# Kernel tuning notes

Measured on AMD Instinct MI355X. Metric: run time of the kernel, lower is better.

Reference implementation:

```python
import jax, jax.numpy as jnp
import numpy as np

N = 100000       # nodes
F_IN = 1433      # input features (Cora)
HID = 67         # hidden dim (hardcoded in module)
C = 7            # classes (Cora)
E = 3200000      # edges (avg degree 32)


def setup_inputs() -> dict:
    key = jax.random.key(0)
    k = jax.random.split(key, 4)
    x = jax.random.normal(k[0], (N, F_IN), dtype=jnp.float32)
    edge_index = jax.random.randint(k[1], (2, E), 0, N, dtype=jnp.int32)
    W1 = jax.random.normal(k[2], (F_IN, HID), dtype=jnp.float32) / np.float32(np.sqrt(F_IN))
    b1 = jnp.zeros((HID,), dtype=jnp.float32)
    W2 = jax.random.normal(k[3], (HID, C), dtype=jnp.float32) / np.float32(np.sqrt(HID))
    b2 = jnp.zeros((C,), dtype=jnp.float32)
    return {"x": x, "edge_index": edge_index, "W1": W1, "b1": b1, "W2": W2, "b2": b2}


def gcn_conv(x, edge_index, W, b):
    """PyG GCNConv: h = W x; out = D^-1/2 (A + I) D^-1/2 h + b."""
    n = x.shape[0]
    h = x @ W  # [n, out_dim]
    loops = jnp.arange(n, dtype=edge_index.dtype)
    row = jnp.concatenate([edge_index[0], loops])  # source
    col = jnp.concatenate([edge_index[1], loops])  # target
    deg = jax.ops.segment_sum(jnp.ones_like(col, dtype=h.dtype), col, num_segments=n)
    dinv = jnp.where(deg > 0, jax.lax.rsqrt(deg), jnp.float32(0))
    norm = dinv[row] * dinv[col]                    # [E+n]
    msg = h[row] * norm[:, None]                    # gather + scale
    out = jax.ops.segment_sum(msg, col, num_segments=n)  # scatter-add
    return out + b


def reference(x, edge_index, W1, b1, W2, b2):
    h = gcn_conv(x, edge_index, W1, b1)
    h = jax.nn.leaky_relu(h, negative_slope=0.01)
    # F.dropout(p=0.951, training=self.training) -> identity in eval mode
    h = gcn_conv(h, edge_index, W2, b2)
    return jax.nn.log_softmax(h, axis=1)
```

## Files before the change

### kernel.cpp

```cpp
#include <hip/hip_runtime.h>
#include <math.h>

#define FIN  1433
#define HID  67
#define HIDP 68
#define NC   7
#define NCP  8

#define BK     32
#define KTILES 45
#define KPAD   (KTILES*BK)
#define COLP   80

typedef __attribute__((ext_vector_type(8))) short short8;
typedef __attribute__((ext_vector_type(4))) float floatx4;

static __device__ inline unsigned short f2bf(float f) {
    unsigned int u = __float_as_uint(f);
    unsigned int r = (u + 0x7fffu + ((u >> 16) & 1u)) >> 16;
    return (unsigned short)r;
}


__global__ void k_zero(int* __restrict__ cnt, int N) {
    int i = blockIdx.x * 256 + threadIdx.x;
    if (i < N) cnt[i] = 0;
}

__global__ void k_count(const int* __restrict__ dst, int* __restrict__ cnt, int E) {
    int e = blockIdx.x * 256 + threadIdx.x;
    if (e < E) atomicAdd(&cnt[dst[e]], 1);
}

__global__ void k_bsum(const int* __restrict__ cnt, int* __restrict__ bsum, int N) {
    __shared__ int s[256];
    int t = threadIdx.x;
    int i = blockIdx.x * 256 + t;
    s[t] = (i < N) ? cnt[i] : 0;
    __syncthreads();
    for (int o = 128; o > 0; o >>= 1) {
        if (t < o) s[t] += s[t + o];
        __syncthreads();
    }
    if (t == 0) bsum[blockIdx.x] = s[0];
}

__global__ void k_scanb(int* __restrict__ bsum, int nb) {
    __shared__ int s[512];
    int t = threadIdx.x;
    int v = (t < nb) ? bsum[t] : 0;
    s[t] = v;
    __syncthreads();
    for (int o = 1; o < 512; o <<= 1) {
        int tmp = (t >= o) ? s[t - o] : 0;
        __syncthreads();
        s[t] += tmp;
        __syncthreads();
    }
    if (t < nb) bsum[t] = s[t] - v;
}

__global__ void k_scan3(const int* __restrict__ cnt, const int* __restrict__ bsum,
                        int* __restrict__ rowptr, int* __restrict__ cursor,
                        float* __restrict__ dinv, int N, int E) {
    __shared__ int s[256];
    int t = threadIdx.x;
    int i = blockIdx.x * 256 + t;
    int v = (i < N) ? cnt[i] : 0;
    s[t] = v;
    __syncthreads();
    for (int o = 1; o < 256; o <<= 1) {
        int tmp = (t >= o) ? s[t - o] : 0;
        __syncthreads();
        s[t] += tmp;
        __syncthreads();
    }
    if (i < N) {
        int start = bsum[blockIdx.x] + s[t] - v;
        rowptr[i] = start;
        cursor[i] = start;
        dinv[i]   = rsqrtf((float)(v + 1));
    }
    if (i == 0) rowptr[N] = E;
}

__global__ void k_fill(const int* __restrict__ ei, int* __restrict__ cursor,
                       int* __restrict__ csrs, int E) {
    int e = blockIdx.x * 256 + threadIdx.x;
    if (e < E) {
        int s = ei[e];
        int d = ei[E + e];
        int pos = atomicAdd(&cursor[d], 1);
        csrs[pos] = s;
    }
}


__global__ void k_wcvt(const float* __restrict__ W1, const float* __restrict__ x,
                       unsigned short* __restrict__ Wt, float* __restrict__ xpad, int N) {
    int idx = blockIdx.x * 256 + threadIdx.x;
    if (idx < KPAD) xpad[idx] = (idx < FIN) ? x[(long long)(N - 1) * FIN + idx] : 0.f;
    if (idx >= COLP * KPAD) return;
    int col = idx / KPAD;
    int k   = idx - col * KPAD;
    float v = (col < HID && k < FIN) ? W1[k * HID + col] : 0.f;
    Wt[idx] = f2bf(v);
}


#define GEMM1_LOAD(Abuf, KT) do {                       \
        __builtin_memcpy(&Abuf[0], xp0 + (KT), 32);     \
        __builtin_memcpy(&Abuf[8], xp1 + (KT), 32);     \
    } while (0)

#define GEMM1_STEP(Abuf, KT) do {                                                   \
        short8 fa0, fa1;                                                            \
        _Pragma("unroll")                                                           \
        for (int u = 0; u < 8; u++) {                                               \
            fa0[u] = (short)f2bf(Abuf[u]);                                          \
            fa1[u] = (short)f2bf(Abuf[8 + u]);                                      \
        }                                                                           \
        _Pragma("unroll")                                                           \
        for (int j = 0; j < 5; j++) {                                               \
            short8 bf = *(const short8*)(wb + j * 16 * KPAD + (KT));                \
            acc0[j] = __builtin_amdgcn_mfma_f32_16x16x32_bf16(fa0, bf, acc0[j], 0, 0, 0); \
            acc1[j] = __builtin_amdgcn_mfma_f32_16x16x32_bf16(fa1, bf, acc1[j], 0, 0, 0); \
        }                                                                           \
    } while (0)

__global__ __launch_bounds__(256) void k_gemm1(const float* __restrict__ x,
                                               const unsigned short* __restrict__ Wt,
                                               const float* __restrict__ dinv,
                                               const float* __restrict__ xpad,
                                               float* __restrict__ h1s, int N) {
    int t    = threadIdx.x;
    int lane = t & 63;
    int w    = t >> 6;
    int lm   = lane & 15;
    int lq   = lane >> 4;
    int row0w = blockIdx.x * 128 + w * 32;

    int r0 = row0w + lm;
    int r1 = row0w + 16 + lm;
    const float* xp0 = (r0 >= N - 1) ? xpad : (x + (long long)r0 * FIN);
    const float* xp1 = (r1 >= N - 1) ? xpad : (x + (long long)r1 * FIN);
    xp0 += lq * 8;
    xp1 += lq * 8;
    const unsigned short* wb = Wt + lm * KPAD + lq * 8;

    floatx4 acc0[5], acc1[5];
#pragma unroll
    for (int j = 0; j < 5; j++) {
        acc0[j] = (floatx4){0.f, 0.f, 0.f, 0.f};
        acc1[j] = (floatx4){0.f, 0.f, 0.f, 0.f};
    }

    float A0[16], A1[16];
    GEMM1_LOAD(A0, 0);
    int kt = 0;
    for (; kt + 2 * BK < KPAD; kt += 2 * BK) {
        GEMM1_LOAD(A1, kt + BK);
        GEMM1_STEP(A0, kt);
        GEMM1_LOAD(A0, kt + 2 * BK);
        GEMM1_STEP(A1, kt + BK);
    }
    GEMM1_STEP(A0, kt);

#pragma unroll
    for (int i = 0; i < 4; i++) {
        int row = row0w + lq * 4 + i;
        if (row < N) {
            float dv = dinv[row];
            long long off = (long long)row * HIDP;
#pragma unroll
            for (int j = 0; j < 5; j++) {
                int col = j * 16 + lm;
                if (col < HIDP) h1s[off + col] = dv * acc0[j][i];
            }
        }
        int row2 = row0w + 16 + lq * 4 + i;
        if (row2 < N) {
            float dv = dinv[row2];
            long long off = (long long)row2 * HIDP;
#pragma unroll
            for (int j = 0; j < 5; j++) {
                int col = j * 16 + lm;
                if (col < HIDP) h1s[off + col] = dv * acc1[j][i];
            }
        }
    }
}


__global__ __launch_bounds__(256) void k_agg1(const float* __restrict__ h1s,
                                              const int* __restrict__ rowptr,
                                              const int* __restrict__ csrs,
                                              const float* __restrict__ dinv,
                                              const float* __restrict__ bias1,
                                              float* __restrict__ out1, int N) {
    int lane = threadIdx.x & 63;
    int d = blockIdx.x * 4 + (threadIdx.x >> 6);
    if (d >= N) return;
    int start = rowptr[d];
    int end   = rowptr[d + 1];
    int tl = 64 + (lane & 3);

    float m0 = 0.f, m1 = 0.f, m2 = 0.f, m3 = 0.f;
    float t0 = 0.f, t1 = 0.f, t2 = 0.f, t3 = 0.f;
    int e = start;
    for (; e + 4 <= end; e += 4) {
        int s0 = csrs[e], s1 = csrs[e + 1], s2 = csrs[e + 2], s3 = csrs[e + 3];
        const float* p0 = h1s + (long long)s0 * HIDP;
        const float* p1 = h1s + (long long)s1 * HIDP;
        const float* p2 = h1s + (long long)s2 * HIDP;
        const float* p3 = h1s + (long long)s3 * HIDP;
        m0 += p0[lane];  t0 += p0[tl];
        m1 += p1[lane];  t1 += p1[tl];
        m2 += p2[lane];  t2 += p2[tl];
        m3 += p3[lane];  t3 += p3[tl];
    }
    for (; e < end; e++) {
        const float* p = h1s + (long long)csrs[e] * HIDP;
        m0 += p[lane];
        t0 += p[tl];
    }
    float dd = dinv[d];
    const float* pd = h1s + (long long)d * HIDP;
    float sa = ((m0 + m1) + (m2 + m3)) + pd[lane];
    float sb = ((t0 + t1) + (t2 + t3)) + pd[tl];
    float vm = bias1[lane] + dd * sa;
    out1[(long long)d * HIDP + lane] = vm > 0.f ? vm : 0.01f * vm;
    if (lane < 4) {
        int j = 64 + lane;
        float bb = (j < HID) ? bias1[j] : 0.f;
        float vt = bb + dd * sb;
        out1[(long long)d * HIDP + j] = vt > 0.f ? vt : 0.01f * vt;
    }
}


__global__ __launch_bounds__(256) void k_gemm2(const float* __restrict__ out1,
                                               const float* __restrict__ W2,
                                               const float* __restrict__ dinv,
                                               float* __restrict__ h2s, int N) {
    __shared__ float w2s[HIDP][NCP];
    int t = threadIdx.x;
    for (int idx = t; idx < HIDP * NCP; idx += 256) {
        int k = idx >> 3, j = idx & 7;
        w2s[k][j] = (k < HID && j < NC) ? W2[k * NC + j] : 0.f;
    }
    __syncthreads();
    int i = blockIdx.x * 256 + t;
    if (i >= N) return;
    const float4* row = (const float4*)(out1 + (long long)i * HIDP);
    float acc[NC];
#pragma unroll
    for (int j = 0; j < NC; j++) acc[j] = 0.f;
#pragma unroll
    for (int kq = 0; kq < 17; kq++) {
        float4 v = row[kq];
        float av[4] = {v.x, v.y, v.z, v.w};
#pragma unroll
        for (int c = 0; c < 4; c++) {
            int k = kq * 4 + c;
            float a = av[c];
#pragma unroll
            for (int j = 0; j < NC; j++) acc[j] = fmaf(a, w2s[k][j], acc[j]);
        }
    }
    float dv = dinv[i];
    float* hp = h2s + (long long)i * NCP;
#pragma unroll
    for (int j = 0; j < NC; j++) hp[j] = dv * acc[j];
    hp[NC] = 0.f;
}


__global__ __launch_bounds__(256) void k_agg2(const float* __restrict__ h2s,
                                              const int* __restrict__ rowptr,
                                              const int* __restrict__ csrs,
                                              const float* __restrict__ dinv,
                                              const float* __restrict__ b2,
                                              float* __restrict__ out, int N) {
    int lane = threadIdx.x & 63;
    int d = blockIdx.x * 4 + (threadIdx.x >> 6);
    if (d >= N) return;
    int es = lane >> 3;
    int j  = lane & 7;
    int start = rowptr[d], end = rowptr[d + 1];
    float acc = 0.f;
    for (int e = start + es; e < end; e += 8) {
        int s = csrs[e];
        acc += h2s[(long long)s * NCP + j];
    }
#pragma unroll
    for (int o = 32; o >= 8; o >>= 1) acc += __shfl_xor(acc, o);
    float dd = dinv[d];
    float self = h2s[(long long)d * NCP + j];
    float v = ((j < NC) ? b2[j] : 0.f) + dd * (self + acc);
    float mv = (j == NC) ? -1e30f : v;
#pragma unroll
    for (int o = 4; o >= 1; o >>= 1) mv = fmaxf(mv, __shfl_xor(mv, o));
    float ex = (j == NC) ? 0.f : __expf(v - mv);
    float ss = ex;
#pragma unroll
    for (int o = 4; o >= 1; o >>= 1) ss += __shfl_xor(ss, o);
    if (lane < 8 && j < NC) {
        out[(long long)d * NC + j] = v - mv - __logf(ss);
    }
}


extern "C" void kernel_launch(void* const* d_in, const int* in_sizes, int n_in,
                              void* d_out, int out_size, void* d_ws, size_t ws_size,
                              hipStream_t stream) {
    const float* x  = (const float*)d_in[0];
    const int*   ei = (const int*)d_in[1];
    const float* W1 = (const float*)d_in[2];
    const float* b1 = (const float*)d_in[3];
    const float* W2 = (const float*)d_in[4];
    const float* b2 = (const float*)d_in[5];
    float* out = (float*)d_out;

    int N = in_sizes[0] / FIN;
    int E = in_sizes[1] / 2;

    size_t o = 0;
    auto alloc = [&](size_t words) { size_t r = o; o += words; o = (o + 63) & ~(size_t)63; return r; };
    size_t o_dinv   = alloc((size_t)N);
    size_t o_cnt    = alloc((size_t)N);
    size_t o_rowptr = alloc((size_t)N + 1);
    size_t o_cursor = alloc((size_t)N);
    size_t o_bsum   = alloc(1024);
    size_t o_csrs   = alloc((size_t)E);
    size_t o_wt     = alloc((size_t)COLP * KPAD / 2);
    size_t o_xpad   = alloc((size_t)KPAD);
    size_t o_h1s    = alloc((size_t)N * HIDP);
    size_t o_out1   = alloc((size_t)N * HIDP);
    size_t o_h2s    = alloc((size_t)N * NCP);

    float* wsf = (float*)d_ws;
    int*   wsi = (int*)d_ws;
    float* dinv   = wsf + o_dinv;
    int*   cnt    = wsi + o_cnt;
    int*   rowptr = wsi + o_rowptr;
    int*   cursor = wsi + o_cursor;
    int*   bsum   = wsi + o_bsum;
    int*   csrs   = wsi + o_csrs;
    unsigned short* Wt = (unsigned short*)(wsi + o_wt);
    float* xpad   = wsf + o_xpad;
    float* h1s    = wsf + o_h1s;
    float* o1     = wsf + o_out1;
    float* h2s    = wsf + o_h2s;

    int nb = (N + 255) / 256;
    int eb = (E + 255) / 256;
    int gb = (N + 127) / 128;

    k_zero <<<nb, 256, 0, stream>>>(cnt, N);
    k_count<<<eb, 256, 0, stream>>>(ei + E, cnt, E);
    k_bsum <<<nb, 256, 0, stream>>>(cnt, bsum, N);
    k_scanb<<<1, 512, 0, stream>>>(bsum, nb);
    k_scan3<<<nb, 256, 0, stream>>>(cnt, bsum, rowptr, cursor, dinv, N, E);
    k_fill <<<eb, 256, 0, stream>>>(ei, cursor, csrs, E);

    k_wcvt <<<(COLP * KPAD + 255) / 256, 256, 0, stream>>>(W1, x, Wt, xpad, N);
    k_gemm1<<<gb, 256, 0, stream>>>(x, Wt, dinv, xpad, h1s, N);
    k_agg1 <<<(N + 3) / 4, 256, 0, stream>>>(h1s, rowptr, csrs, dinv, b1, o1, N);
    k_gemm2<<<nb, 256, 0, stream>>>(o1, W2, dinv, h2s, N);
    k_agg2 <<<(N + 3) / 4, 256, 0, stream>>>(h2s, rowptr, csrs, dinv, b2, out, N);
}
```

Measured before the change: 1.454 ms.

## Fuse second GEMM into aggregation, split hidden layout, shrink GEMM1 tile

The second linear layer (67x7) is folded into the first aggregation kernel through a wave-wide shuffle reduction. This removes the k_gemm2 launch and the write and re-read of the N x 68 intermediate. The hidden features are split into a 64-wide array and a 4-wide array so that each gathered row is a 256-byte aligned access. GEMM1 now handles 16 rows per wave instead of 32, which halves register use but no longer shares each B-fragment load across two MFMAs. The 64-bit index arithmetic is replaced with 32-bit int, and the 7x6 shuffle reduction adds per-node work in agg1.

```diff
diff --git a/kernel.cpp b/kernel.cpp
--- a/kernel.cpp
+++ b/kernel.cpp
@@ -3,7 +3,6 @@
 
 #define FIN  1433
 #define HID  67
-#define HIDP 68
 #define NC   7
 #define NCP  8
 
@@ -99,7 +98,7 @@
 __global__ void k_wcvt(const float* __restrict__ W1, const float* __restrict__ x,
                        unsigned short* __restrict__ Wt, float* __restrict__ xpad, int N) {
     int idx = blockIdx.x * 256 + threadIdx.x;
-    if (idx < KPAD) xpad[idx] = (idx < FIN) ? x[(long long)(N - 1) * FIN + idx] : 0.f;
+    if (idx < KPAD) xpad[idx] = (idx < FIN) ? x[(N - 1) * FIN + idx] : 0.f;
     if (idx >= COLP * KPAD) return;
     int col = idx / KPAD;
     int k   = idx - col * KPAD;
@@ -108,23 +107,16 @@
 }
 
 
-#define GEMM1_LOAD(Abuf, KT) do {                       \
-        __builtin_memcpy(&Abuf[0], xp0 + (KT), 32);     \
-        __builtin_memcpy(&Abuf[8], xp1 + (KT), 32);     \
-    } while (0)
+#define GEMM1_LOAD(Abuf, KT) __builtin_memcpy(&Abuf[0], xp0 + (KT), 32)
 
 #define GEMM1_STEP(Abuf, KT) do {                                                   \
-        short8 fa0, fa1;                                                            \
+        short8 fa;                                                                  \
         _Pragma("unroll")                                                           \
-        for (int u = 0; u < 8; u++) {                                               \
-            fa0[u] = (short)f2bf(Abuf[u]);                                          \
-            fa1[u] = (short)f2bf(Abuf[8 + u]);                                      \
-        }                                                                           \
+        for (int u = 0; u < 8; u++) fa[u] = (short)f2bf(Abuf[u]);                   \
         _Pragma("unroll")                                                           \
         for (int j = 0; j < 5; j++) {                                               \
             short8 bf = *(const short8*)(wb + j * 16 * KPAD + (KT));                \
-            acc0[j] = __builtin_amdgcn_mfma_f32_16x16x32_bf16(fa0, bf, acc0[j], 0, 0, 0); \
-            acc1[j] = __builtin_amdgcn_mfma_f32_16x16x32_bf16(fa1, bf, acc1[j], 0, 0, 0); \
+            acc[j] = __builtin_amdgcn_mfma_f32_16x16x32_bf16(fa, bf, acc[j], 0, 0, 0); \
         }                                                                           \
     } while (0)
 
@@ -132,30 +124,25 @@
                                                const unsigned short* __restrict__ Wt,
                                                const float* __restrict__ dinv,
                                                const float* __restrict__ xpad,
-                                               float* __restrict__ h1s, int N) {
+                                               float* __restrict__ h64,
+                                               float* __restrict__ h4, int N) {
     int t    = threadIdx.x;
     int lane = t & 63;
     int w    = t >> 6;
     int lm   = lane & 15;
     int lq   = lane >> 4;
-    int row0w = blockIdx.x * 128 + w * 32;
+    int row0w = blockIdx.x * 64 + w * 16;
 
     int r0 = row0w + lm;
-    int r1 = row0w + 16 + lm;
-    const float* xp0 = (r0 >= N - 1) ? xpad : (x + (long long)r0 * FIN);
-    const float* xp1 = (r1 >= N - 1) ? xpad : (x + (long long)r1 * FIN);
+    const float* xp0 = (r0 >= N - 1) ? xpad : (x + r0 * FIN);
     xp0 += lq * 8;
-    xp1 += lq * 8;
     const unsigned short* wb = Wt + lm * KPAD + lq * 8;
 
-    floatx4 acc0[5], acc1[5];
-#pragma unroll
-    for (int j = 0; j < 5; j++) {
-        acc0[j] = (floatx4){0.f, 0.f, 0.f, 0.f};
-        acc1[j] = (floatx4){0.f, 0.f, 0.f, 0.f};
-    }
-
-    float A0[16], A1[16];
+    floatx4 acc[5];
+#pragma unroll
+    for (int j = 0; j < 5; j++) acc[j] = (floatx4){0.f, 0.f, 0.f, 0.f};
+
+    float A0[8], A1[8];
     GEMM1_LOAD(A0, 0);
     int kt = 0;
     for (; kt + 2 * BK < KPAD; kt += 2 * BK) {
@@ -171,108 +158,74 @@
         int row = row0w + lq * 4 + i;
         if (row < N) {
             float dv = dinv[row];
-            long long off = (long long)row * HIDP;
-#pragma unroll
-            for (int j = 0; j < 5; j++) {
-                int col = j * 16 + lm;
-                if (col < HIDP) h1s[off + col] = dv * acc0[j][i];
-            }
+            int off = row * 64;
+#pragma unroll
+            for (int j = 0; j < 4; j++) h64[off + j * 16 + lm] = dv * acc[j][i];
+            if (lm < 4) h4[row * 4 + lm] = dv * acc[4][i];
         }
-        int row2 = row0w + 16 + lq * 4 + i;
-        if (row2 < N) {
-            float dv = dinv[row2];
-            long long off = (long long)row2 * HIDP;
-#pragma unroll
-            for (int j = 0; j < 5; j++) {
-                int col = j * 16 + lm;
-                if (col < HIDP) h1s[off + col] = dv * acc1[j][i];
-            }
-        }
-    }
-}
-
-
-__global__ __launch_bounds__(256) void k_agg1(const float* __restrict__ h1s,
+    }
+}
+
+
+__global__ __launch_bounds__(256) void k_agg1(const float* __restrict__ h64,
+                                              const float* __restrict__ h4,
                                               const int* __restrict__ rowptr,
                                               const int* __restrict__ csrs,
                                               const float* __restrict__ dinv,
                                               const float* __restrict__ bias1,
-                                              float* __restrict__ out1, int N) {
+                                              const float* __restrict__ W2,
+                                              float* __restrict__ h2s, int N) {
     int lane = threadIdx.x & 63;
     int d = blockIdx.x * 4 + (threadIdx.x >> 6);
     if (d >= N) return;
     int start = rowptr[d];
     int end   = rowptr[d + 1];
-    int tl = 64 + (lane & 3);
+    int tc = lane & 3;
 
     float m0 = 0.f, m1 = 0.f, m2 = 0.f, m3 = 0.f;
     float t0 = 0.f, t1 = 0.f, t2 = 0.f, t3 = 0.f;
     int e = start;
     for (; e + 4 <= end; e += 4) {
         int s0 = csrs[e], s1 = csrs[e + 1], s2 = csrs[e + 2], s3 = csrs[e + 3];
-        const float* p0 = h1s + (long long)s0 * HIDP;
-        const float* p1 = h1s + (long long)s1 * HIDP;
-        const float* p2 = h1s + (long long)s2 * HIDP;
-        const float* p3 = h1s + (long long)s3 * HIDP;
-        m0 += p0[lane];  t0 += p0[tl];
-        m1 += p1[lane];  t1 += p1[tl];
-        m2 += p2[lane];  t2 += p2[tl];
-        m3 += p3[lane];  t3 += p3[tl];
+        m0 += h64[s0 * 64 + lane];  t0 += h4[s0 * 4 + tc];
+        m1 += h64[s1 * 64 + lane];  t1 += h4[s1 * 4 + tc];
+        m2 += h64[s2 * 64 + lane];  t2 += h4[s2 * 4 + tc];
+        m3 += h64[s3 * 64 + lane];  t3 += h4[s3 * 4 + tc];
     }
     for (; e < end; e++) {
-        const float* p = h1s + (long long)csrs[e] * HIDP;
-        m0 += p[lane];
-        t0 += p[tl];
+        int s = csrs[e];
+        m0 += h64[s * 64 + lane];
+        t0 += h4[s * 4 + tc];
     }
     float dd = dinv[d];
-    const float* pd = h1s + (long long)d * HIDP;
-    float sa = ((m0 + m1) + (m2 + m3)) + pd[lane];
-    float sb = ((t0 + t1) + (t2 + t3)) + pd[tl];
+    float sa = ((m0 + m1) + (m2 + m3)) + h64[d * 64 + lane];
+    float sb = ((t0 + t1) + (t2 + t3)) + h4[d * 4 + tc];
+
     float vm = bias1[lane] + dd * sa;
-    out1[(long long)d * HIDP + lane] = vm > 0.f ? vm : 0.01f * vm;
-    if (lane < 4) {
-        int j = 64 + lane;
-        float bb = (j < HID) ? bias1[j] : 0.f;
-        float vt = bb + dd * sb;
-        out1[(long long)d * HIDP + j] = vt > 0.f ? vt : 0.01f * vt;
-    }
-}
-
-
-__global__ __launch_bounds__(256) void k_gemm2(const float* __restrict__ out1,
-                                               const float* __restrict__ W2,
-                                               const float* __restrict__ dinv,
-                                               float* __restrict__ h2s, int N) {
-    __shared__ float w2s[HIDP][NCP];
-    int t = threadIdx.x;
-    for (int idx = t; idx < HIDP * NCP; idx += 256) {
-        int k = idx >> 3, j = idx & 7;
-        w2s[k][j] = (k < HID && j < NC) ? W2[k * NC + j] : 0.f;
-    }
-    __syncthreads();
-    int i = blockIdx.x * 256 + t;
-    if (i >= N) return;
-    const float4* row = (const float4*)(out1 + (long long)i * HIDP);
-    float acc[NC];
-#pragma unroll
-    for (int j = 0; j < NC; j++) acc[j] = 0.f;
-#pragma unroll
-    for (int kq = 0; kq < 17; kq++) {
-        float4 v = row[kq];
-        float av[4] = {v.x, v.y, v.z, v.w};
-#pragma unroll
-        for (int c = 0; c < 4; c++) {
-            int k = kq * 4 + c;
-            float a = av[c];
-#pragma unroll
-            for (int j = 0; j < NC; j++) acc[j] = fmaf(a, w2s[k][j], acc[j]);
-        }
-    }
-    float dv = dinv[i];
-    float* hp = h2s + (long long)i * NCP;
-#pragma unroll
-    for (int j = 0; j < NC; j++) hp[j] = dv * acc[j];
-    hp[NC] = 0.f;
+    vm = vm > 0.f ? vm : 0.01f * vm;
+    int tcol = 64 + tc;
+    float bb = (tcol < HID) ? bias1[tcol] : 0.f;
+    float vt = bb + dd * sb;
+    vt = vt > 0.f ? vt : 0.01f * vt;
+
+    float pj[NC];
+#pragma unroll
+    for (int j = 0; j < NC; j++) {
+        float wm = W2[lane * NC + j];
+        float wt = (lane < 3) ? W2[(64 + lane) * NC + j] : 0.f;
+        pj[j] = vm * wm + vt * wt;
+    }
+#pragma unroll
+    for (int o = 32; o >= 1; o >>= 1) {
+#pragma unroll
+        for (int j = 0; j < NC; j++) pj[j] += __shfl_xor(pj[j], o);
+    }
+    if (lane == 0) {
+        int off = d * NCP;
+#pragma unroll
+        for (int j = 0; j < NC; j++) h2s[off + j] = dd * pj[j];
+        h2s[off + NC] = 0.f;
+    }
 }
 
 
@@ -291,12 +244,12 @@
     float acc = 0.f;
     for (int e = start + es; e < end; e += 8) {
         int s = csrs[e];
-        acc += h2s[(long long)s * NCP + j];
+        acc += h2s[s * NCP + j];
     }
 #pragma unroll
     for (int o = 32; o >= 8; o >>= 1) acc += __shfl_xor(acc, o);
     float dd = dinv[d];
-    float self = h2s[(long long)d * NCP + j];
+    float self = h2s[d * NCP + j];
     float v = ((j < NC) ? b2[j] : 0.f) + dd * (self + acc);
     float mv = (j == NC) ? -1e30f : v;
 #pragma unroll
@@ -306,7 +259,7 @@
 #pragma unroll
     for (int o = 4; o >= 1; o >>= 1) ss += __shfl_xor(ss, o);
     if (lane < 8 && j < NC) {
-        out[(long long)d * NC + j] = v - mv - __logf(ss);
+        out[d * NC + j] = v - mv - __logf(ss);
     }
 }
 
@@ -335,8 +288,8 @@
     size_t o_csrs   = alloc((size_t)E);
     size_t o_wt     = alloc((size_t)COLP * KPAD / 2);
     size_t o_xpad   = alloc((size_t)KPAD);
-    size_t o_h1s    = alloc((size_t)N * HIDP);
-    size_t o_out1   = alloc((size_t)N * HIDP);
+    size_t o_h64    = alloc((size_t)N * 64);
+    size_t o_h4     = alloc((size_t)N * 4);
     size_t o_h2s    = alloc((size_t)N * NCP);
 
     float* wsf = (float*)d_ws;
@@ -349,13 +302,13 @@
     int*   csrs   = wsi + o_csrs;
     unsigned short* Wt = (unsigned short*)(wsi + o_wt);
     float* xpad   = wsf + o_xpad;
-    float* h1s    = wsf + o_h1s;
-    float* o1     = wsf + o_out1;
+    float* h64    = wsf + o_h64;
+    float* h4     = wsf + o_h4;
     float* h2s    = wsf + o_h2s;
 
     int nb = (N + 255) / 256;
     int eb = (E + 255) / 256;
-    int gb = (N + 127) / 128;
+    int gb = (N + 63) / 64;
 
     k_zero <<<nb, 256, 0, stream>>>(cnt, N);
     k_count<<<eb, 256, 0, stream>>>(ei + E, cnt, E);
@@ -365,8 +318,7 @@
     k_fill <<<eb, 256, 0, stream>>>(ei, cursor, csrs, E);
 
     k_wcvt <<<(COLP * KPAD + 255) / 256, 256, 0, stream>>>(W1, x, Wt, xpad, N);
-    k_gemm1<<<gb, 256, 0, stream>>>(x, Wt, dinv, xpad, h1s, N);
-    k_agg1 <<<(N + 3) / 4, 256, 0, stream>>>(h1s, rowptr, csrs, dinv, b1, o1, N);
-    k_gemm2<<<nb, 256, 0, stream>>>(o1, W2, dinv, h2s, N);
+    k_gemm1<<<gb, 256, 0, stream>>>(x, Wt, dinv, xpad, h64, h4, N);
+    k_agg1 <<<(N + 3) / 4, 256, 0, stream>>>(h64, h4, rowptr, csrs, dinv, b1, W2, h2s, N);
     k_agg2 <<<(N + 3) / 4, 256, 0, stream>>>(h2s, rowptr, csrs, dinv, b2, out, N);
 }
```

Result: no change. 1.466 ms (+0.8%).
